# Kernel tuning notes

Measured on AMD Instinct MI355X. Metric: run time of the kernel, lower is better.

Reference implementation:

```python
import jax, jax.numpy as jnp
import numpy as np


def setup_inputs() -> dict:
    key = jax.random.key(0)
    k_x, k_w1, k_b1, k_w2, k_b2 = jax.random.split(key, 5)
    N, D, H = 4_000_000, 10, 16
    x = jax.random.normal(k_x, (N, D), dtype=jnp.float32)
    # torch.nn.Linear default init: U(-1/sqrt(fan_in), 1/sqrt(fan_in))
    lim1 = 1.0 / np.sqrt(D)
    W1 = jax.random.uniform(k_w1, (H, D), minval=-lim1, maxval=lim1, dtype=jnp.float32)
    b1 = jax.random.uniform(k_b1, (H,), minval=-lim1, maxval=lim1, dtype=jnp.float32)
    lim2 = 1.0 / np.sqrt(H)
    W2 = jax.random.uniform(k_w2, (1, H), minval=-lim2, maxval=lim2, dtype=jnp.float32)
    b2 = jax.random.uniform(k_b2, (1,), minval=-lim2, maxval=lim2, dtype=jnp.float32)
    return {"x": x, "W1": W1, "b1": b1, "W2": W2, "b2": b2}


def reference(x, W1, b1, W2, b2):
    # Gram matrix: (10, 10)
    y = x.T @ x
    # symmetric eigendecomposition; w: eigenvectors (10, 10), ascending eigenvalues
    v, w = jnp.linalg.eigh(y)
    h = jax.nn.relu(w @ W1.T + b1)          # (10, 16)
    o = h @ W2.T + b2                        # (10, 1)
    return 0.5 * (jax.nn.sigmoid(o) + 1.0)
```

## Files before the change

### kernel.cpp

```cpp
#include <hip/hip_runtime.h>
#include <math.h>

#pragma clang fp contract(off)

#define NACC 55
#define KC_DEFAULT 384
#define FOLD_LDS 12288

__device__ __forceinline__ void group_load(const float4* __restrict__ xv,
                                           long g, float4* buf) {
#pragma unroll
  for (int t = 0; t < 20; ++t) buf[t] = xv[g * 20 + t];
}

__device__ __forceinline__ void pair_fma_one(const float4 q0, const float4 q1,
                                             const float4 q2, const float4 q3,
                                             const float4 q4, float* acc) {
  float a[10] = {q0.x, q0.y, q0.z, q0.w, q1.x, q1.y, q1.z, q1.w, q2.x, q2.y};
  float b[10] = {q2.z, q2.w, q3.x, q3.y, q3.z, q3.w, q4.x, q4.y, q4.z, q4.w};
  int e = 0;
#pragma unroll
  for (int i = 0; i < 10; ++i)
#pragma unroll
    for (int j = 0; j <= i; ++j) {
      acc[e] = __builtin_fmaf(a[i], a[j], acc[e]);
      acc[e] = __builtin_fmaf(b[i], b[j], acc[e]);
      ++e;
    }
}

__device__ __forceinline__ void group_fma(const float4* buf, float* acc) {
#pragma unroll
  for (int pp = 0; pp < 4; ++pp)
    pair_fma_one(buf[pp * 5 + 0], buf[pp * 5 + 1], buf[pp * 5 + 2],
                 buf[pp * 5 + 3], buf[pp * 5 + 4], acc);
}

__global__ __launch_bounds__(64, 1) void gram32_kernel(
    const float* __restrict__ x, float* __restrict__ partial,
    int nrows, int kc, int nchunks, int prow) {
  int c = blockIdx.x * 64 + threadIdx.x;
  if (c >= nchunks) return;
  long k0 = (long)c * kc;
  long rem = (long)nrows - k0;
  int klen = rem < kc ? (int)rem : kc;

  float acc[NACC];
#pragma unroll
  for (int e = 0; e < NACC; ++e) acc[e] = 0.0f;

  const float4* __restrict__ xv = (const float4*)(x + k0 * 10);
  int npair = klen >> 1;
  int ngrp = npair >> 2;

  float4 bufA[20], bufB[20];

  int g = 0;
  if (ngrp > 0) group_load(xv, 0, bufA);
  while (g < ngrp) {
    if (g + 1 < ngrp) group_load(xv, g + 1, bufB);
    group_fma(bufA, acc);
    ++g;
    if (g >= ngrp) break;
    if (g + 1 < ngrp) group_load(xv, g + 1, bufA);
    group_fma(bufB, acc);
    ++g;
  }
  for (int p = ngrp * 4; p < npair; ++p) {
    float4 v0 = xv[(long)p * 5 + 0];
    float4 v1 = xv[(long)p * 5 + 1];
    float4 v2 = xv[(long)p * 5 + 2];
    float4 v3 = xv[(long)p * 5 + 3];
    float4 v4 = xv[(long)p * 5 + 4];
    pair_fma_one(v0, v1, v2, v3, v4, acc);
  }
  if (klen & 1) {
    const float* row = x + (k0 + klen - 1) * 10;
    float a[10];
#pragma unroll
    for (int i = 0; i < 10; ++i) a[i] = row[i];
    int e = 0;
#pragma unroll
    for (int i = 0; i < 10; ++i)
#pragma unroll
      for (int j = 0; j <= i; ++j) {
        acc[e] = __builtin_fmaf(a[i], a[j], acc[e]);
        ++e;
      }
  }
#pragma unroll
  for (int e = 0; e < NACC; ++e)
    partial[(long)e * prow + c] = acc[e];
}

__global__ __launch_bounds__(256) void fold32_kernel(
    const float* __restrict__ partial, float* __restrict__ G, int nchunks,
    int prow) {
  __shared__ float buf[FOLD_LDS];
  int e = blockIdx.x;
  const float* p = partial + (long)e * prow;

  if (nchunks <= FOLD_LDS) {
    int n4 = nchunks >> 2;
    const float4* p4 = (const float4*)p;
    float4* b4 = (float4*)buf;
    for (int i = threadIdx.x; i < n4; i += 256) b4[i] = p4[i];
    for (int i = (n4 << 2) + threadIdx.x; i < nchunks; i += 256)
      buf[i] = p[i];
    __syncthreads();
    if (threadIdx.x == 0) {
      float s = buf[0];
      int c = 1;
      for (; c + 16 <= nchunks; c += 16) {
        float v[16];
#pragma unroll
        for (int t = 0; t < 16; ++t) v[t] = buf[c + t];
#pragma unroll
        for (int t = 0; t < 16; ++t) s = s + v[t];
      }
      for (; c < nchunks; ++c) s = s + buf[c];
      G[e] = s;
    }
  } else {
    if (threadIdx.x == 0) {
      float s = p[0];
      for (int c = 1; c < nchunks; ++c) s = s + p[c];
      G[e] = s;
    }
  }
}

__device__ __forceinline__ float s_sign(float a, float b) {
  return copysignf(fabsf(a), b);
}
__device__ __forceinline__ float slapy2(float x, float y) {
  float xa = fabsf(x), ya = fabsf(y);
  float w = fmaxf(xa, ya), z = fminf(xa, ya);
  if (z == 0.0f) return w;
  float t = z / w;
  return w * sqrtf(1.0f + t * t);
}
__device__ __forceinline__ void slartg(float f, float g, float* c, float* s,
                                       float* r) {
  if (g == 0.0f) {
    *c = 1.0f; *s = 0.0f; *r = f;
  } else if (f == 0.0f) {
    *c = 0.0f; *s = s_sign(1.0f, g); *r = fabsf(g);
  } else {
    float d = sqrtf(f * f + g * g);
    *c = fabsf(f) / d;
    *r = s_sign(d, f);
    *s = g / (*r);
  }
}
__device__ void slaev2(float a, float b, float c, float* rt1, float* rt2,
                       float* cs1, float* sn1) {
  float sm = a + c, df = a - c;
  float adf = fabsf(df);
  float tb = b + b;
  float ab = fabsf(tb);
  float acmx, acmn;
  if (fabsf(a) > fabsf(c)) { acmx = a; acmn = c; } else { acmx = c; acmn = a; }
  float rt;
  if (adf > ab) { float t = ab / adf; rt = adf * sqrtf(1.0f + t * t); }
  else if (adf < ab) { float t = adf / ab; rt = ab * sqrtf(1.0f + t * t); }
  else rt = ab * sqrtf(2.0f);
  int sgn1;
  if (sm < 0.0f) {
    *rt1 = 0.5f * (sm - rt); sgn1 = -1;
    *rt2 = (acmx / *rt1) * acmn - (b / *rt1) * b;
  } else if (sm > 0.0f) {
    *rt1 = 0.5f * (sm + rt); sgn1 = 1;
    *rt2 = (acmx / *rt1) * acmn - (b / *rt1) * b;
  } else {
    *rt1 = 0.5f * rt; *rt2 = -0.5f * rt; sgn1 = 1;
  }
  int sgn2;
  float cs;
  if (df >= 0.0f) { cs = df + rt; sgn2 = 1; } else { cs = df - rt; sgn2 = -1; }
  float acs = fabsf(cs);
  if (acs > ab) {
    float ct = -tb / cs;
    *sn1 = 1.0f / sqrtf(1.0f + ct * ct);
    *cs1 = ct * (*sn1);
  } else {
    if (ab == 0.0f) { *cs1 = 1.0f; *sn1 = 0.0f; }
    else {
      float tn = -cs / tb;
      *cs1 = 1.0f / sqrtf(1.0f + tn * tn);
      *sn1 = tn * (*cs1);
    }
  }
  if (sgn1 == sgn2) { float tn = *cs1; *cs1 = -(*sn1); *sn1 = tn; }
}

#define GETD(i) ((i)==0?d0:(i)==1?d1:(i)==2?d2:(i)==3?d3:(i)==4?d4:(i)==5?d5:(i)==6?d6:(i)==7?d7:(i)==8?d8:d9)
#define PUTD(i,v) do{int _i=(i);float _x=(v);d0=(_i==0)?_x:d0;d1=(_i==1)?_x:d1;d2=(_i==2)?_x:d2;d3=(_i==3)?_x:d3;d4=(_i==4)?_x:d4;d5=(_i==5)?_x:d5;d6=(_i==6)?_x:d6;d7=(_i==7)?_x:d7;d8=(_i==8)?_x:d8;d9=(_i==9)?_x:d9;}while(0)
#define GETE(i) ((i)==0?e0:(i)==1?e1:(i)==2?e2:(i)==3?e3:(i)==4?e4:(i)==5?e5:(i)==6?e6:(i)==7?e7:e8)
#define PUTE(i,v) do{int _i=(i);float _x=(v);e0=(_i==0)?_x:e0;e1=(_i==1)?_x:e1;e2=(_i==2)?_x:e2;e3=(_i==3)?_x:e3;e4=(_i==4)?_x:e4;e5=(_i==5)?_x:e5;e6=(_i==6)?_x:e6;e7=(_i==7)?_x:e7;e8=(_i==8)?_x:e8;}while(0)
#define GETWC(i) ((i)==0?wc0:(i)==1?wc1:(i)==2?wc2:(i)==3?wc3:(i)==4?wc4:(i)==5?wc5:(i)==6?wc6:(i)==7?wc7:wc8)
#define PUTWC(i,v) do{int _i=(i);float _x=(v);wc0=(_i==0)?_x:wc0;wc1=(_i==1)?_x:wc1;wc2=(_i==2)?_x:wc2;wc3=(_i==3)?_x:wc3;wc4=(_i==4)?_x:wc4;wc5=(_i==5)?_x:wc5;wc6=(_i==6)?_x:wc6;wc7=(_i==7)?_x:wc7;wc8=(_i==8)?_x:wc8;}while(0)
#define GETWS(i) ((i)==0?ws0:(i)==1?ws1:(i)==2?ws2:(i)==3?ws3:(i)==4?ws4:(i)==5?ws5:(i)==6?ws6:(i)==7?ws7:ws8)
#define PUTWS(i,v) do{int _i=(i);float _x=(v);ws0=(_i==0)?_x:ws0;ws1=(_i==1)?_x:ws1;ws2=(_i==2)?_x:ws2;ws3=(_i==3)?_x:ws3;ws4=(_i==4)?_x:ws4;ws5=(_i==5)?_x:ws5;ws6=(_i==6)?_x:ws6;ws7=(_i==7)?_x:ws7;ws8=(_i==8)?_x:ws8;}while(0)
#define GETZ(i) ((i)==0?z0:(i)==1?z1:(i)==2?z2:(i)==3?z3:(i)==4?z4:(i)==5?z5:(i)==6?z6:(i)==7?z7:(i)==8?z8:z9)
#define PUTZ(i,v) do{int _i=(i);float _x=(v);z0=(_i==0)?_x:z0;z1=(_i==1)?_x:z1;z2=(_i==2)?_x:z2;z3=(_i==3)?_x:z3;z4=(_i==4)?_x:z4;z5=(_i==5)?_x:z5;z6=(_i==6)?_x:z6;z7=(_i==7)?_x:z7;z8=(_i==8)?_x:z8;z9=(_i==9)?_x:z9;}while(0)

__global__ __launch_bounds__(64, 1) void solve_kernel(
    const float* __restrict__ Gp, const float* __restrict__ W1,
    const float* __restrict__ b1, const float* __restrict__ W2,
    const float* __restrict__ b2, float* __restrict__ out) {
  const int lane = threadIdx.x;
  const int myrow = lane < 10 ? lane : 9;

  float row[10];
#pragma unroll
  for (int c = 0; c < 10; ++c) {
    int rr = myrow >= c ? myrow : c;
    int cc = myrow >= c ? c : myrow;
    row[c] = Gp[rr * (rr + 1) / 2 + cc];
  }

  float d0, d1, d2, d3, d4, d5, d6, d7, d8, d9;
  float e0, e1, e2, e3, e4, e5, e6, e7, e8;
  float tau[9];

#pragma unroll
  for (int i = 0; i < 9; ++i) {
    float v[10];
    {
      float myci = row[i];
#pragma unroll
      for (int k = 0; k < 10; ++k) v[k] = __shfl(myci, k, 64);
    }
    float alpha = v[i + 1];
    float xn2 = 0.0f;
#pragma unroll
    for (int k = i + 2; k < 10; ++k) xn2 = xn2 + v[k] * v[k];
    float xnorm = sqrtf(xn2);
    float taui;
    if (xnorm == 0.0f) {
      taui = 0.0f;
      PUTE(i, alpha);
    } else {
      float beta = -s_sign(slapy2(alpha, xnorm), alpha);
      taui = (beta - alpha) / beta;
      float sc = 1.0f / (alpha - beta);
#pragma unroll
      for (int k = i + 2; k < 10; ++k) v[k] = v[k] * sc;
      if (lane >= i + 2 && lane < 10) row[i] = row[i] * sc;
      if (lane == i) {
#pragma unroll
        for (int c = i + 2; c < 10; ++c) row[c] = row[c] * sc;
      }
      if (lane == i + 1) row[i] = beta;
      if (lane == i) row[i + 1] = beta;
      PUTE(i, beta);
    }
    if (taui != 0.0f) {
      v[i + 1] = 1.0f;
      float vme = (lane == i + 1)
                      ? 1.0f
                      : ((lane >= i + 2 && lane < 10) ? row[i] : 0.0f);
      float s = 0.0f;
#pragma unroll
      for (int c2 = i + 1; c2 < 10; ++c2) s = s + row[c2] * v[c2];
      float pvr = taui * s;
      float pva[10];
#pragma unroll
      for (int k = 0; k < 10; ++k) pva[k] = __shfl(pvr, k, 64);
      float dot = 0.0f;
#pragma unroll
      for (int k = i + 1; k < 10; ++k) dot = dot + pva[k] * v[k];
      float alpha2 = -0.5f * taui * dot;
      pvr = pvr + alpha2 * vme;
#pragma unroll
      for (int k = 0; k < 10; ++k) pva[k] = pva[k] + alpha2 * v[k];
      if (lane >= i + 1 && lane < 10) {
#pragma unroll
        for (int c2 = i + 1; c2 < 10; ++c2)
          row[c2] = row[c2] - (vme * pva[c2] + pvr * v[c2]);
      }
    }
    tau[i] = taui;
    PUTD(i, __shfl(row[i], i, 64));
  }
  PUTD(9, __shfl(row[9], 9, 64));

  float z0, z1, z2, z3, z4, z5, z6, z7, z8, z9;
  z0 = (lane == 0) ? 1.0f : 0.0f;
  z1 = (lane == 1) ? 1.0f : 0.0f;
  z2 = (lane == 2) ? 1.0f : 0.0f;
  z3 = (lane == 3) ? 1.0f : 0.0f;
  z4 = (lane == 4) ? 1.0f : 0.0f;
  z5 = (lane == 5) ? 1.0f : 0.0f;
  z6 = (lane == 6) ? 1.0f : 0.0f;
  z7 = (lane == 7) ? 1.0f : 0.0f;
  z8 = (lane == 8) ? 1.0f : 0.0f;
  z9 = (lane == 9) ? 1.0f : 0.0f;

  float wc0, wc1, wc2, wc3, wc4, wc5, wc6, wc7, wc8;
  float ws0, ws1, ws2, ws3, ws4, ws5, ws6, ws7, ws8;
  wc0 = wc1 = wc2 = wc3 = wc4 = wc5 = wc6 = wc7 = wc8 = 0.0f;
  ws0 = ws1 = ws2 = ws3 = ws4 = ws5 = ws6 = ws7 = ws8 = 0.0f;

  const float eps = 5.9604644775390625e-08f;
  const float eps2 = 3.5527136788005009e-15f;
  const float safmin = 1.1754943508222875e-38f;
  const int nmaxit = 300;
  int jtot = 0;
  int l1 = 0;

  while (l1 < 10) {
    if (l1 > 0) PUTE(l1 - 1, 0.0f);
    int m = 9;
    {
      bool fnd = false;
#pragma unroll
      for (int mm = 0; mm < 9; ++mm) {
        if (!fnd && mm >= l1) {
          float tst = fabsf(GETE(mm));
          if (tst == 0.0f) {
            m = mm; fnd = true;
          } else if (tst <=
                     (sqrtf(fabsf(GETD(mm))) * sqrtf(fabsf(GETD(mm + 1)))) *
                         eps) {
            PUTE(mm, 0.0f); m = mm; fnd = true;
          }
        }
      }
    }
    int l = l1, lsv = l, lend = m, lendsv = lend;
    l1 = m + 1;
    if (lend == l) continue;
    float anorm = 0.0f;
#pragma unroll
    for (int k = 0; k < 10; ++k)
      if (k >= l && k <= lend) anorm = fmaxf(anorm, fabsf(GETD(k)));
#pragma unroll
    for (int k = 0; k < 9; ++k)
      if (k >= l && k < lend) anorm = fmaxf(anorm, fabsf(GETE(k)));
    if (anorm == 0.0f) continue;
    if (fabsf(GETD(lend)) < fabsf(GETD(l))) { lend = lsv; l = lendsv; }

    if (lend > l) {
      for (;;) {
        int m2 = lend;
        if (l != lend) {
          bool fnd = false;
#pragma unroll
          for (int mm = 0; mm < 9; ++mm) {
            if (!fnd && mm >= l && mm <= lend - 1) {
              float tst = GETE(mm) * GETE(mm);
              if (tst <=
                  (eps2 * fabsf(GETD(mm))) * fabsf(GETD(mm + 1)) + safmin) {
                m2 = mm; fnd = true;
              }
            }
          }
        }
        if (m2 < lend) PUTE(m2, 0.0f);
        float p = GETD(l);
        if (m2 == l) {
          ++l;
          if (l <= lend) continue;
          break;
        }
        if (m2 == l + 1) {
          float rt1, rt2, cc2, ss2;
          slaev2(GETD(l), GETE(l), GETD(l + 1), &rt1, &rt2, &cc2, &ss2);
          {
            float zl = GETZ(l), zl1 = GETZ(l + 1);
            float t = zl1;
            float nl1 = cc2 * t - ss2 * zl;
            float nl = ss2 * t + cc2 * zl;
            PUTZ(l + 1, nl1);
            PUTZ(l, nl);
          }
          PUTD(l, rt1);
          PUTD(l + 1, rt2);
          PUTE(l, 0.0f);
          l += 2;
          if (l <= lend) continue;
          break;
        }
        if (jtot == nmaxit) break;
        ++jtot;
        float g = (GETD(l + 1) - p) / (2.0f * GETE(l));
        float r2 = slapy2(g, 1.0f);
        g = GETD(m2) - p + (GETE(l) / (g + s_sign(r2, g)));
        float ss = 1.0f, cc = 1.0f;
        p = 0.0f;
#pragma unroll
        for (int i2 = 8; i2 >= 0; --i2) {
          if (i2 >= l && i2 <= m2 - 1) {
            float f = ss * GETE(i2);
            float bb = cc * GETE(i2);
            slartg(g, f, &cc, &ss, &r2);
            if (i2 != m2 - 1) PUTE(i2 + 1, r2);
            g = GETD(i2 + 1) - p;
            r2 = (GETD(i2) - g) * ss + 2.0f * cc * bb;
            p = ss * r2;
            PUTD(i2 + 1, g + p);
            g = cc * r2 - bb;
            PUTWC(i2, cc);
            PUTWS(i2, -ss);
          }
        }
#pragma unroll
        for (int j = 8; j >= 0; --j) {
          if (j >= l && j <= m2 - 1) {
            float cj = GETWC(j), sj = GETWS(j);
            float t = GETZ(j + 1);
            float zj = GETZ(j);
            PUTZ(j + 1, cj * t - sj * zj);
            PUTZ(j, sj * t + cj * zj);
          }
        }
        PUTD(l, GETD(l) - p);
        PUTE(l, g);
      }
    } else {
      for (;;) {
        int m2 = lend;
        if (l != lend) {
          bool fnd = false;
#pragma unroll
          for (int mm = 9; mm >= 1; --mm) {
            if (!fnd && mm <= l && mm >= lend + 1) {
              float tst = GETE(mm - 1) * GETE(mm - 1);
              if (tst <=
                  (eps2 * fabsf(GETD(mm))) * fabsf(GETD(mm - 1)) + safmin) {
                m2 = mm; fnd = true;
              }
            }
          }
        }
        if (m2 > lend) PUTE(m2 - 1, 0.0f);
        float p = GETD(l);
        if (m2 == l) {
          --l;
          if (l >= lend) continue;
          break;
        }
        if (m2 == l - 1) {
          float rt1, rt2, cc2, ss2;
          slaev2(GETD(l - 1), GETE(l - 1), GETD(l), &rt1, &rt2, &cc2, &ss2);
          {
            float zl = GETZ(l), zlm = GETZ(l - 1);
            float t = zl;
            float nl = cc2 * t - ss2 * zlm;
            float nlm = ss2 * t + cc2 * zlm;
            PUTZ(l, nl);
            PUTZ(l - 1, nlm);
          }
          PUTD(l - 1, rt1);
          PUTD(l, rt2);
          PUTE(l - 1, 0.0f);
          l -= 2;
          if (l >= lend) continue;
          break;
        }
        if (jtot == nmaxit) break;
        ++jtot;
        float g = (GETD(l - 1) - p) / (2.0f * GETE(l - 1));
        float r2 = slapy2(g, 1.0f);
        g = GETD(m2) - p + (GETE(l - 1) / (g + s_sign(r2, g)));
        float ss = 1.0f, cc = 1.0f;
        p = 0.0f;
#pragma unroll
        for (int i2 = 0; i2 <= 8; ++i2) {
          if (i2 >= m2 && i2 <= l - 1) {
            float f = ss * GETE(i2);
            float bb = cc * GETE(i2);
            slartg(g, f, &cc, &ss, &r2);
            if (i2 != m2) PUTE(i2 - 1, r2);
            g = GETD(i2) - p;
            r2 = (GETD(i2 + 1) - g) * ss + 2.0f * cc * bb;
            p = ss * r2;
            PUTD(i2, g + p);
            g = cc * r2 - bb;
            PUTWC(i2, cc);
            PUTWS(i2, ss);
          }
        }
#pragma unroll
        for (int j = 0; j <= 8; ++j) {
          if (j >= m2 && j <= l - 1) {
            float cj = GETWC(j), sj = GETWS(j);
            float t = GETZ(j + 1);
            float zj = GETZ(j);
            PUTZ(j + 1, cj * t - sj * zj);
            PUTZ(j, sj * t + cj * zj);
          }
        }
        PUTD(l, GETD(l) - p);
        PUTE(l - 1, g);
      }
    }
  }

#pragma unroll
  for (int ii = 1; ii < 10; ++ii) {
    const int i2 = ii - 1;
    int k2 = i2;
    float pmin = GETD(i2);
#pragma unroll
    for (int j = ii; j < 10; ++j) {
      float dj = GETD(j);
      if (dj < pmin) { k2 = j; pmin = dj; }
    }
    if (k2 != i2) {
      PUTD(k2, GETD(i2));
      PUTD(i2, pmin);
      float ti = GETZ(i2);
      float tk = GETZ(k2);
      PUTZ(i2, tk);
      PUTZ(k2, ti);
    }
  }

  float zc[10];
#pragma unroll
  for (int r = 0; r < 10; ++r) zc[r] = 0.0f;
  {
    float zreg[10] = {z0, z1, z2, z3, z4, z5, z6, z7, z8, z9};
#pragma unroll
    for (int r = 0; r < 10; ++r) {
#pragma unroll
      for (int c = 0; c < 10; ++c) {
        float t = __shfl(zreg[c], r, 64);
        zc[r] = (lane == c) ? t : zc[r];
      }
    }
  }

#pragma unroll
  for (int i = 8; i >= 0; --i) {
    float taui = tau[i];
    if (taui != 0.0f) {
      float hv[10];
      {
        float myci = row[i];
#pragma unroll
        for (int k = 0; k < 10; ++k) hv[k] = __shfl(myci, k, 64);
      }
      float w = zc[i + 1];
#pragma unroll
      for (int k2 = i + 2; k2 < 10; ++k2) w = w + hv[k2] * zc[k2];
      w = w * taui;
      zc[i + 1] = zc[i + 1] - w;
#pragma unroll
      for (int k2 = i + 2; k2 < 10; ++k2) zc[k2] = zc[k2] - hv[k2] * w;
    }
  }

  float zrow[10];
#pragma unroll
  for (int c = 0; c < 10; ++c) zrow[c] = 0.0f;
#pragma unroll
  for (int r = 0; r < 10; ++r) {
#pragma unroll
    for (int c = 0; c < 10; ++c) {
      float t = __shfl(zc[r], c, 64);
      zrow[c] = (lane == r) ? t : zrow[c];
    }
  }

  if (lane < 10) {
    float o = 0.0f;
#pragma unroll
    for (int j = 0; j < 16; ++j) {
      float acc = 0.0f;
#pragma unroll
      for (int k = 0; k < 10; ++k) acc = acc + zrow[k] * W1[j * 10 + k];
      acc = acc + b1[j];
      float h = fmaxf(acc, 0.0f);
      o = o + h * W2[j];
    }
    o = o + b2[0];
    float sig = 1.0f / (1.0f + expf(-o));
    out[lane] = 0.5f * (sig + 1.0f);
  }
}

extern "C" void kernel_launch(void* const* d_in, const int* in_sizes, int n_in,
                              void* d_out, int out_size, void* d_ws,
                              size_t ws_size, hipStream_t stream) {
  const float* x = (const float*)d_in[0];
  const float* W1 = (const float*)d_in[1];
  const float* b1 = (const float*)d_in[2];
  const float* W2 = (const float*)d_in[3];
  const float* b2 = (const float*)d_in[4];
  float* out = (float*)d_out;

  int nrows = in_sizes[0] / 10;

  int kc = KC_DEFAULT;
  for (;;) {
    long nchunks = ((long)nrows + kc - 1) / kc;
    long prow = (nchunks + 63) & ~63L;
    size_t need = (size_t)NACC * prow * sizeof(float) + 256;
    if (need <= ws_size || kc > nrows) break;
    kc *= 2;
  }
  int nchunks = (int)(((long)nrows + kc - 1) / kc);
  int prow = (int)(((long)nchunks + 63) & ~63L);

  float* partial = (float*)d_ws;
  float* G = partial + (size_t)NACC * prow;

  int grid = (nchunks + 63) / 64;
  gram32_kernel<<<grid, 64, 0, stream>>>(x, partial, nrows, kc, nchunks,
                                         prow);
  fold32_kernel<<<NACC, 256, 0, stream>>>(partial, G, nchunks, prow);
  solve_kernel<<<1, 64, 0, stream>>>(G, W1, b1, W2, b2, out);
}
```

Measured before the change: 181.9 us.

## Distribute tridiagonal QL state across lanes with shuffles and ballots

Replaces the per-thread scalar copies of the diagonal, off-diagonal and rotation arrays (accessed through long select chains) with one value per lane, read back via __shfl. Convergence searches become wave-wide ballot plus ctz/clz, the norm becomes a shuffle-xor max reduction, and the rotation loops run only over the active range with unrolling disabled. The aim is to cut the heavy select-chain instruction count and register pressure in the single-wave eigen solver. In exchange, each loop step now carries shuffle latency and loop control.

```diff
diff --git a/kernel.cpp b/kernel.cpp
--- a/kernel.cpp
+++ b/kernel.cpp
@@ -196,12 +196,6 @@
 
 #define GETD(i) ((i)==0?d0:(i)==1?d1:(i)==2?d2:(i)==3?d3:(i)==4?d4:(i)==5?d5:(i)==6?d6:(i)==7?d7:(i)==8?d8:d9)
 #define PUTD(i,v) do{int _i=(i);float _x=(v);d0=(_i==0)?_x:d0;d1=(_i==1)?_x:d1;d2=(_i==2)?_x:d2;d3=(_i==3)?_x:d3;d4=(_i==4)?_x:d4;d5=(_i==5)?_x:d5;d6=(_i==6)?_x:d6;d7=(_i==7)?_x:d7;d8=(_i==8)?_x:d8;d9=(_i==9)?_x:d9;}while(0)
-#define GETE(i) ((i)==0?e0:(i)==1?e1:(i)==2?e2:(i)==3?e3:(i)==4?e4:(i)==5?e5:(i)==6?e6:(i)==7?e7:e8)
-#define PUTE(i,v) do{int _i=(i);float _x=(v);e0=(_i==0)?_x:e0;e1=(_i==1)?_x:e1;e2=(_i==2)?_x:e2;e3=(_i==3)?_x:e3;e4=(_i==4)?_x:e4;e5=(_i==5)?_x:e5;e6=(_i==6)?_x:e6;e7=(_i==7)?_x:e7;e8=(_i==8)?_x:e8;}while(0)
-#define GETWC(i) ((i)==0?wc0:(i)==1?wc1:(i)==2?wc2:(i)==3?wc3:(i)==4?wc4:(i)==5?wc5:(i)==6?wc6:(i)==7?wc7:wc8)
-#define PUTWC(i,v) do{int _i=(i);float _x=(v);wc0=(_i==0)?_x:wc0;wc1=(_i==1)?_x:wc1;wc2=(_i==2)?_x:wc2;wc3=(_i==3)?_x:wc3;wc4=(_i==4)?_x:wc4;wc5=(_i==5)?_x:wc5;wc6=(_i==6)?_x:wc6;wc7=(_i==7)?_x:wc7;wc8=(_i==8)?_x:wc8;}while(0)
-#define GETWS(i) ((i)==0?ws0:(i)==1?ws1:(i)==2?ws2:(i)==3?ws3:(i)==4?ws4:(i)==5?ws5:(i)==6?ws6:(i)==7?ws7:ws8)
-#define PUTWS(i,v) do{int _i=(i);float _x=(v);ws0=(_i==0)?_x:ws0;ws1=(_i==1)?_x:ws1;ws2=(_i==2)?_x:ws2;ws3=(_i==3)?_x:ws3;ws4=(_i==4)?_x:ws4;ws5=(_i==5)?_x:ws5;ws6=(_i==6)?_x:ws6;ws7=(_i==7)?_x:ws7;ws8=(_i==8)?_x:ws8;}while(0)
 #define GETZ(i) ((i)==0?z0:(i)==1?z1:(i)==2?z2:(i)==3?z3:(i)==4?z4:(i)==5?z5:(i)==6?z6:(i)==7?z7:(i)==8?z8:z9)
 #define PUTZ(i,v) do{int _i=(i);float _x=(v);z0=(_i==0)?_x:z0;z1=(_i==1)?_x:z1;z2=(_i==2)?_x:z2;z3=(_i==3)?_x:z3;z4=(_i==4)?_x:z4;z5=(_i==5)?_x:z5;z6=(_i==6)?_x:z6;z7=(_i==7)?_x:z7;z8=(_i==8)?_x:z8;z9=(_i==9)?_x:z9;}while(0)
 
@@ -220,8 +214,7 @@
     row[c] = Gp[rr * (rr + 1) / 2 + cc];
   }
 
-  float d0, d1, d2, d3, d4, d5, d6, d7, d8, d9;
-  float e0, e1, e2, e3, e4, e5, e6, e7, e8;
+  float dv = 0.0f, ev = 0.0f;
   float tau[9];
 
 #pragma unroll
@@ -240,7 +233,7 @@
     float taui;
     if (xnorm == 0.0f) {
       taui = 0.0f;
-      PUTE(i, alpha);
+      ev = (lane == i) ? alpha : ev;
     } else {
       float beta = -s_sign(slapy2(alpha, xnorm), alpha);
       taui = (beta - alpha) / beta;
@@ -254,7 +247,7 @@
       }
       if (lane == i + 1) row[i] = beta;
       if (lane == i) row[i + 1] = beta;
-      PUTE(i, beta);
+      ev = (lane == i) ? beta : ev;
     }
     if (taui != 0.0f) {
       v[i + 1] = 1.0f;
@@ -282,9 +275,15 @@
       }
     }
     tau[i] = taui;
-    PUTD(i, __shfl(row[i], i, 64));
-  }
-  PUTD(9, __shfl(row[9], 9, 64));
+    {
+      float t = __shfl(row[i], i, 64);
+      dv = (lane == i) ? t : dv;
+    }
+  }
+  {
+    float t = __shfl(row[9], 9, 64);
+    dv = (lane == 9) ? t : dv;
+  }
 
   float z0, z1, z2, z3, z4, z5, z6, z7, z8, z9;
   z0 = (lane == 0) ? 1.0f : 0.0f;
@@ -298,10 +297,7 @@
   z8 = (lane == 8) ? 1.0f : 0.0f;
   z9 = (lane == 9) ? 1.0f : 0.0f;
 
-  float wc0, wc1, wc2, wc3, wc4, wc5, wc6, wc7, wc8;
-  float ws0, ws1, ws2, ws3, ws4, ws5, ws6, ws7, ws8;
-  wc0 = wc1 = wc2 = wc3 = wc4 = wc5 = wc6 = wc7 = wc8 = 0.0f;
-  ws0 = ws1 = ws2 = ws3 = ws4 = ws5 = ws6 = ws7 = ws8 = 0.0f;
+  float wcv = 0.0f, wsv = 0.0f;
 
   const float eps = 5.9604644775390625e-08f;
   const float eps2 = 3.5527136788005009e-15f;
@@ -311,193 +307,201 @@
   int l1 = 0;
 
   while (l1 < 10) {
-    if (l1 > 0) PUTE(l1 - 1, 0.0f);
+    if (l1 > 0) ev = (lane == l1 - 1) ? 0.0f : ev;
     int m = 9;
     {
-      bool fnd = false;
-#pragma unroll
-      for (int mm = 0; mm < 9; ++mm) {
-        if (!fnd && mm >= l1) {
-          float tst = fabsf(GETE(mm));
-          if (tst == 0.0f) {
-            m = mm; fnd = true;
-          } else if (tst <=
-                     (sqrtf(fabsf(GETD(mm))) * sqrtf(fabsf(GETD(mm + 1)))) *
-                         eps) {
-            PUTE(mm, 0.0f); m = mm; fnd = true;
-          }
-        }
+      float dnx = __shfl(dv, (lane + 1) & 63, 64);
+      float te = fabsf(ev);
+      bool c1 = (te == 0.0f);
+      bool c2 = (te <= (sqrtf(fabsf(dv)) * sqrtf(fabsf(dnx))) * eps);
+      bool inr = (lane >= l1) && (lane <= 8);
+      unsigned long long bal = __ballot(inr && (c1 || c2));
+      if (bal) {
+        m = __builtin_ctzll(bal);
+        ev = ((lane == m) && !c1) ? 0.0f : ev;
       }
     }
     int l = l1, lsv = l, lend = m, lendsv = lend;
     l1 = m + 1;
     if (lend == l) continue;
-    float anorm = 0.0f;
-#pragma unroll
-    for (int k = 0; k < 10; ++k)
-      if (k >= l && k <= lend) anorm = fmaxf(anorm, fabsf(GETD(k)));
-#pragma unroll
-    for (int k = 0; k < 9; ++k)
-      if (k >= l && k < lend) anorm = fmaxf(anorm, fabsf(GETE(k)));
-    if (anorm == 0.0f) continue;
-    if (fabsf(GETD(lend)) < fabsf(GETD(l))) { lend = lsv; l = lendsv; }
+    float va = (lane >= l && lane <= lend) ? fabsf(dv) : 0.0f;
+    float vb = (lane >= l && lane < lend) ? fabsf(ev) : 0.0f;
+    float vm = fmaxf(va, vb);
+#pragma unroll
+    for (int off = 32; off > 0; off >>= 1)
+      vm = fmaxf(vm, __shfl_xor(vm, off, 64));
+    if (vm == 0.0f) continue;
+    {
+      float dle = __shfl(dv, lend, 64);
+      float dls = __shfl(dv, l, 64);
+      if (fabsf(dle) < fabsf(dls)) { lend = lsv; l = lendsv; }
+    }
 
     if (lend > l) {
       for (;;) {
         int m2 = lend;
         if (l != lend) {
-          bool fnd = false;
-#pragma unroll
-          for (int mm = 0; mm < 9; ++mm) {
-            if (!fnd && mm >= l && mm <= lend - 1) {
-              float tst = GETE(mm) * GETE(mm);
-              if (tst <=
-                  (eps2 * fabsf(GETD(mm))) * fabsf(GETD(mm + 1)) + safmin) {
-                m2 = mm; fnd = true;
-              }
-            }
-          }
-        }
-        if (m2 < lend) PUTE(m2, 0.0f);
-        float p = GETD(l);
+          float dnx2 = __shfl(dv, (lane + 1) & 63, 64);
+          float t2 = ev * ev;
+          bool cnd = (t2 <= (eps2 * fabsf(dv)) * fabsf(dnx2) + safmin);
+          bool ir = (lane >= l) && (lane < lend);
+          unsigned long long b2 = __ballot(ir && cnd);
+          if (b2) m2 = __builtin_ctzll(b2);
+        }
+        if (m2 < lend) ev = (lane == m2) ? 0.0f : ev;
+        float p = __shfl(dv, l, 64);
         if (m2 == l) {
           ++l;
           if (l <= lend) continue;
           break;
         }
         if (m2 == l + 1) {
+          float el = __shfl(ev, l, 64);
+          float dl1 = __shfl(dv, l + 1, 64);
           float rt1, rt2, cc2, ss2;
-          slaev2(GETD(l), GETE(l), GETD(l + 1), &rt1, &rt2, &cc2, &ss2);
-          {
-            float zl = GETZ(l), zl1 = GETZ(l + 1);
-            float t = zl1;
-            float nl1 = cc2 * t - ss2 * zl;
-            float nl = ss2 * t + cc2 * zl;
-            PUTZ(l + 1, nl1);
-            PUTZ(l, nl);
-          }
-          PUTD(l, rt1);
-          PUTD(l + 1, rt2);
-          PUTE(l, 0.0f);
+          slaev2(p, el, dl1, &rt1, &rt2, &cc2, &ss2);
+          float zl = GETZ(l), zl1 = GETZ(l + 1);
+          float t = zl1;
+          PUTZ(l + 1, cc2 * t - ss2 * zl);
+          PUTZ(l, ss2 * t + cc2 * zl);
+          dv = (lane == l) ? rt1 : dv;
+          dv = (lane == l + 1) ? rt2 : dv;
+          ev = (lane == l) ? 0.0f : ev;
           l += 2;
           if (l <= lend) continue;
           break;
         }
         if (jtot == nmaxit) break;
         ++jtot;
-        float g = (GETD(l + 1) - p) / (2.0f * GETE(l));
+        float el = __shfl(ev, l, 64);
+        float dl1 = __shfl(dv, l + 1, 64);
+        float dm2 = __shfl(dv, m2, 64);
+        float g = (dl1 - p) / (2.0f * el);
         float r2 = slapy2(g, 1.0f);
-        g = GETD(m2) - p + (GETE(l) / (g + s_sign(r2, g)));
+        g = dm2 - p + (el / (g + s_sign(r2, g)));
         float ss = 1.0f, cc = 1.0f;
         p = 0.0f;
-#pragma unroll
-        for (int i2 = 8; i2 >= 0; --i2) {
-          if (i2 >= l && i2 <= m2 - 1) {
-            float f = ss * GETE(i2);
-            float bb = cc * GETE(i2);
-            slartg(g, f, &cc, &ss, &r2);
-            if (i2 != m2 - 1) PUTE(i2 + 1, r2);
-            g = GETD(i2 + 1) - p;
-            r2 = (GETD(i2) - g) * ss + 2.0f * cc * bb;
-            p = ss * r2;
-            PUTD(i2 + 1, g + p);
-            g = cc * r2 - bb;
-            PUTWC(i2, cc);
-            PUTWS(i2, -ss);
-          }
-        }
-#pragma unroll
-        for (int j = 8; j >= 0; --j) {
-          if (j >= l && j <= m2 - 1) {
-            float cj = GETWC(j), sj = GETWS(j);
-            float t = GETZ(j + 1);
-            float zj = GETZ(j);
-            PUTZ(j + 1, cj * t - sj * zj);
-            PUTZ(j, sj * t + cj * zj);
-          }
-        }
-        PUTD(l, GETD(l) - p);
-        PUTE(l, g);
+#pragma clang loop unroll(disable)
+        for (int i2 = m2 - 1; i2 >= l; --i2) {
+          float ei2 = __shfl(ev, i2, 64);
+          float di2 = __shfl(dv, i2, 64);
+          float di21 = __shfl(dv, i2 + 1, 64);
+          float f = ss * ei2;
+          float bb = cc * ei2;
+          slartg(g, f, &cc, &ss, &r2);
+          if (i2 != m2 - 1) ev = (lane == i2 + 1) ? r2 : ev;
+          g = di21 - p;
+          r2 = (di2 - g) * ss + 2.0f * cc * bb;
+          p = ss * r2;
+          dv = (lane == i2 + 1) ? (g + p) : dv;
+          g = cc * r2 - bb;
+          wcv = (lane == i2) ? cc : wcv;
+          wsv = (lane == i2) ? (-ss) : wsv;
+        }
+        float carry = GETZ(m2);
+#pragma clang loop unroll(disable)
+        for (int j = m2 - 1; j >= l; --j) {
+          float cj = __shfl(wcv, j, 64);
+          float sj = __shfl(wsv, j, 64);
+          float zj = GETZ(j);
+          float t = carry;
+          PUTZ(j + 1, cj * t - sj * zj);
+          carry = sj * t + cj * zj;
+        }
+        PUTZ(l, carry);
+        {
+          float dl0 = __shfl(dv, l, 64);
+          dv = (lane == l) ? (dl0 - p) : dv;
+        }
+        ev = (lane == l) ? g : ev;
       }
     } else {
       for (;;) {
         int m2 = lend;
         if (l != lend) {
-          bool fnd = false;
-#pragma unroll
-          for (int mm = 9; mm >= 1; --mm) {
-            if (!fnd && mm <= l && mm >= lend + 1) {
-              float tst = GETE(mm - 1) * GETE(mm - 1);
-              if (tst <=
-                  (eps2 * fabsf(GETD(mm))) * fabsf(GETD(mm - 1)) + safmin) {
-                m2 = mm; fnd = true;
-              }
-            }
-          }
-        }
-        if (m2 > lend) PUTE(m2 - 1, 0.0f);
-        float p = GETD(l);
+          float epv = __shfl(ev, (lane - 1) & 63, 64);
+          float dpv = __shfl(dv, (lane - 1) & 63, 64);
+          float t2 = epv * epv;
+          bool cnd = (t2 <= (eps2 * fabsf(dv)) * fabsf(dpv) + safmin);
+          bool ir = (lane >= lend + 1) && (lane <= l);
+          unsigned long long b2 = __ballot(ir && cnd);
+          if (b2) m2 = 63 - __builtin_clzll(b2);
+        }
+        if (m2 > lend) ev = (lane == m2 - 1) ? 0.0f : ev;
+        float p = __shfl(dv, l, 64);
         if (m2 == l) {
           --l;
           if (l >= lend) continue;
           break;
         }
         if (m2 == l - 1) {
+          float dlm = __shfl(dv, l - 1, 64);
+          float elm = __shfl(ev, l - 1, 64);
           float rt1, rt2, cc2, ss2;
-          slaev2(GETD(l - 1), GETE(l - 1), GETD(l), &rt1, &rt2, &cc2, &ss2);
-          {
-            float zl = GETZ(l), zlm = GETZ(l - 1);
-            float t = zl;
-            float nl = cc2 * t - ss2 * zlm;
-            float nlm = ss2 * t + cc2 * zlm;
-            PUTZ(l, nl);
-            PUTZ(l - 1, nlm);
-          }
-          PUTD(l - 1, rt1);
-          PUTD(l, rt2);
-          PUTE(l - 1, 0.0f);
+          slaev2(dlm, elm, p, &rt1, &rt2, &cc2, &ss2);
+          float zl = GETZ(l), zlm = GETZ(l - 1);
+          float t = zl;
+          PUTZ(l, cc2 * t - ss2 * zlm);
+          PUTZ(l - 1, ss2 * t + cc2 * zlm);
+          dv = (lane == l - 1) ? rt1 : dv;
+          dv = (lane == l) ? rt2 : dv;
+          ev = (lane == l - 1) ? 0.0f : ev;
           l -= 2;
           if (l >= lend) continue;
           break;
         }
         if (jtot == nmaxit) break;
         ++jtot;
-        float g = (GETD(l - 1) - p) / (2.0f * GETE(l - 1));
+        float elm = __shfl(ev, l - 1, 64);
+        float dlm = __shfl(dv, l - 1, 64);
+        float dm2 = __shfl(dv, m2, 64);
+        float g = (dlm - p) / (2.0f * elm);
         float r2 = slapy2(g, 1.0f);
-        g = GETD(m2) - p + (GETE(l - 1) / (g + s_sign(r2, g)));
+        g = dm2 - p + (elm / (g + s_sign(r2, g)));
         float ss = 1.0f, cc = 1.0f;
         p = 0.0f;
-#pragma unroll
-        for (int i2 = 0; i2 <= 8; ++i2) {
-          if (i2 >= m2 && i2 <= l - 1) {
-            float f = ss * GETE(i2);
-            float bb = cc * GETE(i2);
-            slartg(g, f, &cc, &ss, &r2);
-            if (i2 != m2) PUTE(i2 - 1, r2);
-            g = GETD(i2) - p;
-            r2 = (GETD(i2 + 1) - g) * ss + 2.0f * cc * bb;
-            p = ss * r2;
-            PUTD(i2, g + p);
-            g = cc * r2 - bb;
-            PUTWC(i2, cc);
-            PUTWS(i2, ss);
-          }
-        }
-#pragma unroll
-        for (int j = 0; j <= 8; ++j) {
-          if (j >= m2 && j <= l - 1) {
-            float cj = GETWC(j), sj = GETWS(j);
-            float t = GETZ(j + 1);
-            float zj = GETZ(j);
-            PUTZ(j + 1, cj * t - sj * zj);
-            PUTZ(j, sj * t + cj * zj);
-          }
-        }
-        PUTD(l, GETD(l) - p);
-        PUTE(l - 1, g);
-      }
-    }
-  }
+#pragma clang loop unroll(disable)
+        for (int i2 = m2; i2 <= l - 1; ++i2) {
+          float ei2 = __shfl(ev, i2, 64);
+          float di2 = __shfl(dv, i2, 64);
+          float di21 = __shfl(dv, i2 + 1, 64);
+          float f = ss * ei2;
+          float bb = cc * ei2;
+          slartg(g, f, &cc, &ss, &r2);
+          if (i2 != m2) ev = (lane == i2 - 1) ? r2 : ev;
+          g = di2 - p;
+          r2 = (di21 - g) * ss + 2.0f * cc * bb;
+          p = ss * r2;
+          dv = (lane == i2) ? (g + p) : dv;
+          g = cc * r2 - bb;
+          wcv = (lane == i2) ? cc : wcv;
+          wsv = (lane == i2) ? ss : wsv;
+        }
+        float carry = GETZ(m2);
+#pragma clang loop unroll(disable)
+        for (int j = m2; j <= l - 1; ++j) {
+          float cj = __shfl(wcv, j, 64);
+          float sj = __shfl(wsv, j, 64);
+          float t = GETZ(j + 1);
+          float zj = carry;
+          PUTZ(j, sj * t + cj * zj);
+          carry = cj * t - sj * zj;
+        }
+        PUTZ(l, carry);
+        {
+          float dl0 = __shfl(dv, l, 64);
+          dv = (lane == l) ? (dl0 - p) : dv;
+        }
+        ev = (lane == l - 1) ? g : ev;
+      }
+    }
+  }
+
+  float d0 = __shfl(dv, 0, 64), d1 = __shfl(dv, 1, 64);
+  float d2 = __shfl(dv, 2, 64), d3 = __shfl(dv, 3, 64);
+  float d4 = __shfl(dv, 4, 64), d5 = __shfl(dv, 5, 64);
+  float d6 = __shfl(dv, 6, 64), d7 = __shfl(dv, 7, 64);
+  float d8 = __shfl(dv, 8, 64), d9 = __shfl(dv, 9, 64);
 
 #pragma unroll
   for (int ii = 1; ii < 10; ++ii) {
```

New measurement: 183.9 us. Within noise of the previous version (+1.1%).

## Branchless QL/QR eigen-solver loops and LDS-based transposes in solve kernel

Applied to the files above, without the earlier changes.

Rewrites the tridiagonal QL/QR iteration in the single-wavefront solve kernel to use predicated selects instead of nested branches (slartg, deflation searches, anorm). It also carries the rotated Z component in a register across the rotation loop instead of re-reading it through the GETZ/PUTZ select chains. The 100-shuffle transposes of the eigenvector matrix and Householder vectors are replaced by padded LDS buffers with barriers. The aim is to shorten the serial latency of the tiny eigensolver tail, at the cost of computing both sides of every branch.

```diff
diff --git a/kernel.cpp b/kernel.cpp
--- a/kernel.cpp
+++ b/kernel.cpp
@@ -142,16 +142,15 @@
 }
 __device__ __forceinline__ void slartg(float f, float g, float* c, float* s,
                                        float* r) {
-  if (g == 0.0f) {
-    *c = 1.0f; *s = 0.0f; *r = f;
-  } else if (f == 0.0f) {
-    *c = 0.0f; *s = s_sign(1.0f, g); *r = fabsf(g);
-  } else {
-    float d = sqrtf(f * f + g * g);
-    *c = fabsf(f) / d;
-    *r = s_sign(d, f);
-    *s = g / (*r);
-  }
+  float d = sqrtf(f * f + g * g);
+  float cg = fabsf(f) / d;
+  float rg = s_sign(d, f);
+  float sg = g / rg;
+  bool g0 = (g == 0.0f);
+  bool f0 = (f == 0.0f);
+  *c = g0 ? 1.0f : (f0 ? 0.0f : cg);
+  *s = g0 ? 0.0f : (f0 ? s_sign(1.0f, g) : sg);
+  *r = g0 ? f : (f0 ? fabsf(g) : rg);
 }
 __device__ void slaev2(float a, float b, float c, float* rt1, float* rt2,
                        float* cs1, float* sn1) {
@@ -209,6 +208,8 @@
     const float* __restrict__ Gp, const float* __restrict__ W1,
     const float* __restrict__ b1, const float* __restrict__ W2,
     const float* __restrict__ b2, float* __restrict__ out) {
+  __shared__ float zbuf[10 * 11];
+  __shared__ float abuf[10 * 11];
   const int lane = threadIdx.x;
   const int myrow = lane < 10 ? lane : 9;
 
@@ -316,17 +317,20 @@
     {
       bool fnd = false;
 #pragma unroll
-      for (int mm = 0; mm < 9; ++mm) {
-        if (!fnd && mm >= l1) {
-          float tst = fabsf(GETE(mm));
-          if (tst == 0.0f) {
-            m = mm; fnd = true;
-          } else if (tst <=
-                     (sqrtf(fabsf(GETD(mm))) * sqrtf(fabsf(GETD(mm + 1)))) *
-                         eps) {
-            PUTE(mm, 0.0f); m = mm; fnd = true;
-          }
-        }
+      for (int mm = 0; mm <= 8; ++mm) {
+        float tst = fabsf(GETE(mm));
+        bool c1 = (tst == 0.0f);
+        bool c2 =
+            (tst <= (sqrtf(fabsf(GETD(mm))) * sqrtf(fabsf(GETD(mm + 1)))) *
+                        eps);
+        bool inr = (mm >= l1);
+        bool hit = inr && !fnd && (c1 || c2);
+        {
+          float oldv = GETE(mm);
+          PUTE(mm, (hit && !c1) ? 0.0f : oldv);
+        }
+        m = hit ? mm : m;
+        fnd = fnd || hit;
       }
     }
     int l = l1, lsv = l, lend = m, lendsv = lend;
@@ -334,11 +338,15 @@
     if (lend == l) continue;
     float anorm = 0.0f;
 #pragma unroll
-    for (int k = 0; k < 10; ++k)
-      if (k >= l && k <= lend) anorm = fmaxf(anorm, fabsf(GETD(k)));
-#pragma unroll
-    for (int k = 0; k < 9; ++k)
-      if (k >= l && k < lend) anorm = fmaxf(anorm, fabsf(GETE(k)));
+    for (int k = 0; k <= 9; ++k) {
+      bool in = (k >= l) && (k <= lend);
+      anorm = fmaxf(anorm, in ? fabsf(GETD(k)) : 0.0f);
+    }
+#pragma unroll
+    for (int k = 0; k <= 8; ++k) {
+      bool in = (k >= l) && (k < lend);
+      anorm = fmaxf(anorm, in ? fabsf(GETE(k)) : 0.0f);
+    }
     if (anorm == 0.0f) continue;
     if (fabsf(GETD(lend)) < fabsf(GETD(l))) { lend = lsv; l = lendsv; }
 
@@ -348,14 +356,15 @@
         if (l != lend) {
           bool fnd = false;
 #pragma unroll
-          for (int mm = 0; mm < 9; ++mm) {
-            if (!fnd && mm >= l && mm <= lend - 1) {
-              float tst = GETE(mm) * GETE(mm);
-              if (tst <=
-                  (eps2 * fabsf(GETD(mm))) * fabsf(GETD(mm + 1)) + safmin) {
-                m2 = mm; fnd = true;
-              }
-            }
+          for (int mm = 0; mm <= 8; ++mm) {
+            float tst = GETE(mm) * GETE(mm);
+            bool c =
+                (tst <= (eps2 * fabsf(GETD(mm))) * fabsf(GETD(mm + 1)) +
+                            safmin);
+            bool inr = (mm >= l) && (mm < lend);
+            bool hit = inr && !fnd && c;
+            m2 = hit ? mm : m2;
+            fnd = fnd || hit;
           }
         }
         if (m2 < lend) PUTE(m2, 0.0f);
@@ -367,15 +376,11 @@
         }
         if (m2 == l + 1) {
           float rt1, rt2, cc2, ss2;
-          slaev2(GETD(l), GETE(l), GETD(l + 1), &rt1, &rt2, &cc2, &ss2);
-          {
-            float zl = GETZ(l), zl1 = GETZ(l + 1);
-            float t = zl1;
-            float nl1 = cc2 * t - ss2 * zl;
-            float nl = ss2 * t + cc2 * zl;
-            PUTZ(l + 1, nl1);
-            PUTZ(l, nl);
-          }
+          slaev2(p, GETE(l), GETD(l + 1), &rt1, &rt2, &cc2, &ss2);
+          float zl = GETZ(l), zl1 = GETZ(l + 1);
+          float t = zl1;
+          PUTZ(l + 1, cc2 * t - ss2 * zl);
+          PUTZ(l, ss2 * t + cc2 * zl);
           PUTD(l, rt1);
           PUTD(l + 1, rt2);
           PUTE(l, 0.0f);
@@ -393,10 +398,14 @@
 #pragma unroll
         for (int i2 = 8; i2 >= 0; --i2) {
           if (i2 >= l && i2 <= m2 - 1) {
-            float f = ss * GETE(i2);
-            float bb = cc * GETE(i2);
+            float ei2 = GETE(i2);
+            float f = ss * ei2;
+            float bb = cc * ei2;
             slartg(g, f, &cc, &ss, &r2);
-            if (i2 != m2 - 1) PUTE(i2 + 1, r2);
+            {
+              float oldv = GETE(i2 + 1);
+              PUTE(i2 + 1, (i2 != m2 - 1) ? r2 : oldv);
+            }
             g = GETD(i2 + 1) - p;
             r2 = (GETD(i2) - g) * ss + 2.0f * cc * bb;
             p = ss * r2;
@@ -406,16 +415,18 @@
             PUTWS(i2, -ss);
           }
         }
+        float carry = GETZ(m2);
 #pragma unroll
         for (int j = 8; j >= 0; --j) {
           if (j >= l && j <= m2 - 1) {
             float cj = GETWC(j), sj = GETWS(j);
-            float t = GETZ(j + 1);
             float zj = GETZ(j);
+            float t = carry;
             PUTZ(j + 1, cj * t - sj * zj);
-            PUTZ(j, sj * t + cj * zj);
+            carry = sj * t + cj * zj;
           }
         }
+        PUTZ(l, carry);
         PUTD(l, GETD(l) - p);
         PUTE(l, g);
       }
@@ -426,13 +437,14 @@
           bool fnd = false;
 #pragma unroll
           for (int mm = 9; mm >= 1; --mm) {
-            if (!fnd && mm <= l && mm >= lend + 1) {
-              float tst = GETE(mm - 1) * GETE(mm - 1);
-              if (tst <=
-                  (eps2 * fabsf(GETD(mm))) * fabsf(GETD(mm - 1)) + safmin) {
-                m2 = mm; fnd = true;
-              }
-            }
+            float tst = GETE(mm - 1) * GETE(mm - 1);
+            bool c =
+                (tst <= (eps2 * fabsf(GETD(mm))) * fabsf(GETD(mm - 1)) +
+                            safmin);
+            bool inr = (mm <= l) && (mm >= lend + 1);
+            bool hit = inr && !fnd && c;
+            m2 = hit ? mm : m2;
+            fnd = fnd || hit;
           }
         }
         if (m2 > lend) PUTE(m2 - 1, 0.0f);
@@ -444,15 +456,11 @@
         }
         if (m2 == l - 1) {
           float rt1, rt2, cc2, ss2;
-          slaev2(GETD(l - 1), GETE(l - 1), GETD(l), &rt1, &rt2, &cc2, &ss2);
-          {
-            float zl = GETZ(l), zlm = GETZ(l - 1);
-            float t = zl;
-            float nl = cc2 * t - ss2 * zlm;
-            float nlm = ss2 * t + cc2 * zlm;
-            PUTZ(l, nl);
-            PUTZ(l - 1, nlm);
-          }
+          slaev2(GETD(l - 1), GETE(l - 1), p, &rt1, &rt2, &cc2, &ss2);
+          float zl = GETZ(l), zlm = GETZ(l - 1);
+          float t = zl;
+          PUTZ(l, cc2 * t - ss2 * zlm);
+          PUTZ(l - 1, ss2 * t + cc2 * zlm);
           PUTD(l - 1, rt1);
           PUTD(l, rt2);
           PUTE(l - 1, 0.0f);
@@ -470,10 +478,14 @@
 #pragma unroll
         for (int i2 = 0; i2 <= 8; ++i2) {
           if (i2 >= m2 && i2 <= l - 1) {
-            float f = ss * GETE(i2);
-            float bb = cc * GETE(i2);
+            float ei2 = GETE(i2);
+            float f = ss * ei2;
+            float bb = cc * ei2;
             slartg(g, f, &cc, &ss, &r2);
-            if (i2 != m2) PUTE(i2 - 1, r2);
+            if (i2 >= 1) {
+              float oldv = GETE(i2 - 1);
+              PUTE(i2 - 1, (i2 != m2) ? r2 : oldv);
+            }
             g = GETD(i2) - p;
             r2 = (GETD(i2 + 1) - g) * ss + 2.0f * cc * bb;
             p = ss * r2;
@@ -483,16 +495,18 @@
             PUTWS(i2, ss);
           }
         }
+        float carry = GETZ(m2);
 #pragma unroll
         for (int j = 0; j <= 8; ++j) {
           if (j >= m2 && j <= l - 1) {
             float cj = GETWC(j), sj = GETWS(j);
             float t = GETZ(j + 1);
-            float zj = GETZ(j);
-            PUTZ(j + 1, cj * t - sj * zj);
+            float zj = carry;
             PUTZ(j, sj * t + cj * zj);
+            carry = cj * t - sj * zj;
           }
         }
+        PUTZ(l, carry);
         PUTD(l, GETD(l) - p);
         PUTE(l - 1, g);
       }
@@ -519,31 +533,25 @@
     }
   }
 
+  if (lane < 10) {
+#pragma unroll
+    for (int c = 0; c < 10; ++c) zbuf[lane * 11 + c] = GETZ(c);
+#pragma unroll
+    for (int c = 0; c < 10; ++c) abuf[lane * 11 + c] = row[c];
+  }
+  __syncthreads();
   float zc[10];
 #pragma unroll
-  for (int r = 0; r < 10; ++r) zc[r] = 0.0f;
-  {
-    float zreg[10] = {z0, z1, z2, z3, z4, z5, z6, z7, z8, z9};
-#pragma unroll
-    for (int r = 0; r < 10; ++r) {
-#pragma unroll
-      for (int c = 0; c < 10; ++c) {
-        float t = __shfl(zreg[c], r, 64);
-        zc[r] = (lane == c) ? t : zc[r];
-      }
-    }
-  }
+  for (int r = 0; r < 10; ++r)
+    zc[r] = (lane < 10) ? zbuf[r * 11 + lane] : 0.0f;
 
 #pragma unroll
   for (int i = 8; i >= 0; --i) {
     float taui = tau[i];
     if (taui != 0.0f) {
       float hv[10];
-      {
-        float myci = row[i];
-#pragma unroll
-        for (int k = 0; k < 10; ++k) hv[k] = __shfl(myci, k, 64);
-      }
+#pragma unroll
+      for (int k = 0; k < 10; ++k) hv[k] = abuf[k * 11 + i];
       float w = zc[i + 1];
 #pragma unroll
       for (int k2 = i + 2; k2 < 10; ++k2) w = w + hv[k2] * zc[k2];
@@ -554,17 +562,16 @@
     }
   }
 
+  __syncthreads();
+  if (lane < 10) {
+#pragma unroll
+    for (int r = 0; r < 10; ++r) zbuf[r * 11 + lane] = zc[r];
+  }
+  __syncthreads();
   float zrow[10];
 #pragma unroll
-  for (int c = 0; c < 10; ++c) zrow[c] = 0.0f;
-#pragma unroll
-  for (int r = 0; r < 10; ++r) {
-#pragma unroll
-    for (int c = 0; c < 10; ++c) {
-      float t = __shfl(zc[r], c, 64);
-      zrow[c] = (lane == r) ? t : zrow[c];
-    }
-  }
+  for (int c = 0; c < 10; ++c)
+    zrow[c] = (lane < 10) ? zbuf[lane * 11 + c] : 0.0f;
 
   if (lane < 10) {
     float o = 0.0f;
```

After: 175.0 us. 1.04x faster.
